# Kernel tuning notes

Measured on AMD Instinct MI355X. Metric: run time of the kernel, lower is better.

## Reference

```python
import jax, jax.numpy as jnp
import numpy as np

N, D, H, C = 100000, 128, 8, 16  # nodes, units=H*C, heads, per-head channels
E = 400000                        # edges per edge set (2 edge sets)
LN_EPS = 1e-3                     # keras LayerNormalization default epsilon


def setup_inputs() -> dict:
    key = jax.random.key(0)
    ks = jax.random.split(key, 16)
    def dense(k, i, o):
        return jax.random.normal(k, (i, o), jnp.float32) / np.float32(np.sqrt(i))
    return dict(
        x=jax.random.normal(ks[0], (N, D), jnp.float32),
        src0=jax.random.randint(ks[1], (E,), 0, N),
        dst0=jax.random.randint(ks[2], (E,), 0, N),
        src1=jax.random.randint(ks[3], (E,), 0, N),
        dst1=jax.random.randint(ks[4], (E,), 0, N),
        Wk=dense(ks[5], D, D), bk=jnp.zeros((D,), jnp.float32),
        Wm=dense(ks[6], D, D), bm=jnp.zeros((D,), jnp.float32),
        Wq=dense(ks[7], D, D), bq=jnp.zeros((D,), jnp.float32),
        Wa=dense(ks[8], D, D), ba=jnp.zeros((D,), jnp.float32),
        Watt0=jax.random.normal(ks[9], (H, C, C), jnp.float32) / np.float32(np.sqrt(C)),
        Wmsg0=jax.random.normal(ks[10], (H, C, C), jnp.float32) / np.float32(np.sqrt(C)),
        Watt1=jax.random.normal(ks[11], (H, C, C), jnp.float32) / np.float32(np.sqrt(C)),
        Wmsg1=jax.random.normal(ks[12], (H, C, C), jnp.float32) / np.float32(np.sqrt(C)),
        prior0=jnp.ones((H,), jnp.float32),
        prior1=jnp.ones((H,), jnp.float32),
        skip=jnp.ones((), jnp.float32),
        gamma=jnp.ones((D,), jnp.float32),
        beta=jnp.zeros((D,), jnp.float32),
    )


def reference(x, src0, dst0, src1, dst1, Wk, bk, Wm, bm, Wq, bq, Wa, ba,
              Watt0, Wmsg0, Watt1, Wmsg1, prior0, prior1, skip, gamma, beta):
    # Node-level projections, split per head: [N, H, C]
    k = (x @ Wk + bk).reshape(N, H, C)
    m = (x @ Wm + bm).reshape(N, H, C)
    q = (x @ Wq + bq).reshape(N, H, C)
    scale = 1.0 / jnp.sqrt(jnp.float32(C))

    def edge_terms(src, dst, Watt, Wmsg, prior):
        # per-edge-type relation projections of gathered sender keys/messages
        ke = jnp.einsum('ehk,hkl->ehl', k[src], Watt)          # [E, H, C]
        score = jnp.einsum('ehl,ehl->eh', ke, q[dst]) * prior * scale  # [E, H]
        msg = jnp.einsum('ehk,hkl->ehl', m[src], Wmsg)          # [E, H, C]
        return score, msg

    s0, m0 = edge_terms(src0, dst0, Watt0, Wmsg0, prior0)
    s1, m1 = edge_terms(src1, dst1, Watt1, Wmsg1, prior1)

    # Joint segment softmax over all incoming edges (both edge sets) per receiver
    scores = jnp.concatenate([s0, s1], axis=0)   # [2E, H]
    msgs = jnp.concatenate([m0, m1], axis=0)     # [2E, H, C]
    recv = jnp.concatenate([dst0, dst1], axis=0)

    smax = jax.ops.segment_max(scores, recv, num_segments=N)   # [N, H]
    ex = jnp.exp(scores - smax[recv])
    denom = jax.ops.segment_sum(ex, recv, num_segments=N)      # [N, H]
    d_e = denom[recv]
    attn = ex / jnp.where(d_e > 0, d_e, 1.0)                   # [2E, H]

    pooled = jax.ops.segment_sum(attn[:, :, None] * msgs, recv,
                                 num_segments=N).reshape(N, D)  # [N, D]

    # aggr(gelu(pooled)); weighted skip; layer norm
    h = jax.nn.gelu(pooled, approximate=False) @ Wa + ba
    alpha = jax.nn.sigmoid(skip)
    out = alpha * h + (1.0 - alpha) * x
    mu = jnp.mean(out, axis=-1, keepdims=True)
    var = jnp.var(out, axis=-1, keepdims=True)
    out = (out - mu) * jax.lax.rsqrt(var + LN_EPS) * gamma + beta
    return out
```

## Files before the change

kernel.cpp:

```cpp
#include <hip/hip_runtime.h>
#include <hip/hip_bf16.h>
#include <math.h>

#define N_NODES 100000
#define DIM 128
#define NH 8
#define NC 16
#define E_EDGES 400000
#define LN_EPS 1e-3f
#define SCAN_B 1024

typedef __attribute__((ext_vector_type(8))) short short8v;
typedef __attribute__((ext_vector_type(4))) short short4v;
typedef __attribute__((ext_vector_type(4))) float float4v;

__device__ __forceinline__ short bf16bits(float v) {
    __hip_bfloat16 b = __float2bfloat16(v);
    return *(short*)&b;
}

__global__ __launch_bounds__(128) void fuse_weights(
    const float* __restrict__ Wk, const float* __restrict__ bk,
    const float* __restrict__ Wm, const float* __restrict__ bm,
    const float* __restrict__ Wq, const float* __restrict__ bq,
    const float* __restrict__ Wa, const float* __restrict__ ba,
    const float* __restrict__ Watt0, const float* __restrict__ Wmsg0,
    const float* __restrict__ Watt1, const float* __restrict__ Wmsg1,
    const float* __restrict__ prior0, const float* __restrict__ prior1,
    __hip_bfloat16* __restrict__ Wt, float* __restrict__ bias)
{
    const int c = blockIdx.x;
    const int d = threadIdx.x;
    const int sec = c >> 7, j = c & 127, h = j >> 4, l = j & 15;
    float v, b;
    if (sec == 4)      { v = Wq[d * DIM + j]; b = bq[j]; }
    else if (sec == 5) { v = Wa[d * DIM + j]; b = ba[j]; }
    else {
        const float* W1 = (sec < 2) ? Wk : Wm;
        const float* bs = (sec < 2) ? bk : bm;
        const float* W2 = (sec == 0) ? Watt0 : (sec == 1) ? Watt1
                          : (sec == 2) ? Wmsg0 : Wmsg1;
        float scale = (sec == 0) ? prior0[h] * 0.25f
                    : (sec == 1) ? prior1[h] * 0.25f : 1.f;
        float s = 0.f, sb = 0.f;
        #pragma unroll
        for (int kk = 0; kk < NC; ++kk) {
            float w2 = W2[h * 256 + kk * 16 + l];
            s  = fmaf(W1[d * DIM + h * 16 + kk], w2, s);
            sb = fmaf(bs[h * 16 + kk], w2, sb);
        }
        v = s * scale; b = sb * scale;
    }
    Wt[(size_t)c * DIM + d] = __float2bfloat16(v);
    if (d == 0) bias[c] = b;
}

__global__ __launch_bounds__(256) void proj_mfma(
    const float* __restrict__ x,
    const __hip_bfloat16* __restrict__ Wt,
    const float* __restrict__ bias,
    __hip_bfloat16* __restrict__ kattC,
    __hip_bfloat16* __restrict__ mmsgC,
    __hip_bfloat16* __restrict__ qb)
{
    __shared__ __align__(16) short xs[32 * DIM];
    const int tid = threadIdx.x;
    const int wave = tid >> 6, lane = tid & 63;
    const int quad = lane >> 4, mcol = lane & 15;
    const int r0 = blockIdx.x * 32;

    {
        const int row = tid >> 3, c8 = tid & 7;
        const float* xp = x + (size_t)(r0 + row) * DIM + c8 * 16;
        float4v f[4];
        #pragma unroll
        for (int i = 0; i < 4; ++i) f[i] = *(const float4v*)(xp + i * 4);
        short8v s0, s1;
        #pragma unroll
        for (int j = 0; j < 8; ++j) {
            s0[j] = bf16bits(((const float*)f)[j]);
            s1[j] = bf16bits(((const float*)f)[j + 8]);
        }
        short* base = xs + row * DIM;
        *(short8v*)(base + (((2 * c8)     ^ (row & 7)) * 8)) = s0;
        *(short8v*)(base + (((2 * c8 + 1) ^ (row & 7)) * 8)) = s1;
    }
    __syncthreads();

    short8v b0[4], b1[4];
    #pragma unroll
    for (int kb = 0; kb < 4; ++kb) {
        const int ch = quad + kb * 4;
        b0[kb] = *(const short8v*)(xs + mcol * DIM + ((ch ^ (mcol & 7)) * 8));
        b1[kb] = *(const short8v*)(xs + (mcol + 16) * DIM + ((ch ^ (mcol & 7)) * 8));
    }

    #pragma unroll
    for (int s = 0; s < 5; ++s) {
        __hip_bfloat16* dst =
            (s == 0) ? kattC :
            (s == 1) ? kattC + (size_t)N_NODES * DIM :
            (s == 2) ? mmsgC :
            (s == 3) ? mmsgC + (size_t)N_NODES * DIM :
                       qb;
        short* drow0 = (short*)dst + (size_t)(r0 + mcol) * DIM;
        short* drow1 = drow0 + 16 * DIM;
        #pragma unroll
        for (int tp = 0; tp < 2; ++tp) {
            const int ct = (wave * 2 + tp) * 16;
            const int c0 = s * 128 + ct;
            const short* wp = (const short*)Wt + (size_t)(c0 + mcol) * DIM + quad * 8;
            float4v acc0 = {0.f, 0.f, 0.f, 0.f};
            float4v acc1 = {0.f, 0.f, 0.f, 0.f};
            #pragma unroll
            for (int kb = 0; kb < 4; ++kb) {
                short8v af = *(const short8v*)(wp + kb * 32);
                acc0 = __builtin_amdgcn_mfma_f32_16x16x32_bf16(af, b0[kb], acc0, 0, 0, 0);
                acc1 = __builtin_amdgcn_mfma_f32_16x16x32_bf16(af, b1[kb], acc1, 0, 0, 0);
            }
            const float4v b4 = *(const float4v*)(bias + c0 + quad * 4);
            short4v o0, o1;
            #pragma unroll
            for (int g = 0; g < 4; ++g) {
                o0[g] = bf16bits(acc0[g] + b4[g]);
                o1[g] = bf16bits(acc1[g] + b4[g]);
            }
            *(short4v*)(drow0 + ct + quad * 4) = o0;
            *(short4v*)(drow1 + ct + quad * 4) = o1;
        }
    }
}

__global__ __launch_bounds__(256) void hist_kernel(
    const int* __restrict__ dst0, const int* __restrict__ dst1,
    int* __restrict__ counts)
{
    int e = blockIdx.x * 256 + threadIdx.x;
    if (e < E_EDGES) atomicAdd(&counts[dst0[e]], 1);
    int e1 = e - E_EDGES;
    if (e1 >= 0 && e1 < E_EDGES) atomicAdd(&counts[dst1[e1]], 1);
}

__global__ __launch_bounds__(SCAN_B) void scanA_kernel(
    const int* __restrict__ counts, int* __restrict__ row_ptr,
    int* __restrict__ bsum)
{
    __shared__ int buf[2][SCAN_B];
    int i = blockIdx.x * SCAN_B + threadIdx.x;
    int v = (i < N_NODES) ? counts[i] : 0;
    int cur = 0;
    buf[0][threadIdx.x] = v;
    __syncthreads();
    #pragma unroll
    for (int off = 1; off < SCAN_B; off <<= 1) {
        int t = buf[cur][threadIdx.x];
        int add = (threadIdx.x >= off) ? buf[cur][threadIdx.x - off] : 0;
        buf[cur ^ 1][threadIdx.x] = t + add;
        cur ^= 1;
        __syncthreads();
    }
    int inc = buf[cur][threadIdx.x];
    if (i < N_NODES) row_ptr[i] = inc - v;
    if (threadIdx.x == SCAN_B - 1) bsum[blockIdx.x] = inc;
}

__global__ __launch_bounds__(128) void scanB_kernel(int* __restrict__ bsum, int nblocks)
{
    __shared__ int buf[2][128];
    int t = threadIdx.x;
    int v = (t < nblocks) ? bsum[t] : 0;
    buf[0][t] = v;
    __syncthreads();
    int cur = 0;
    #pragma unroll
    for (int off = 1; off < 128; off <<= 1) {
        int a = buf[cur][t];
        if (t >= off) a += buf[cur][t - off];
        buf[cur ^ 1][t] = a;
        cur ^= 1;
        __syncthreads();
    }
    if (t < nblocks) bsum[t] = buf[cur][t] - v;
}

__global__ __launch_bounds__(SCAN_B) void scanC_kernel(
    int* __restrict__ row_ptr, int* __restrict__ cursor,
    const int* __restrict__ bsum)
{
    int i = blockIdx.x * SCAN_B + threadIdx.x;
    if (i < N_NODES) {
        int r = row_ptr[i] + bsum[blockIdx.x];
        row_ptr[i] = r;
        cursor[i] = r;
    }
}

__global__ __launch_bounds__(256) void scatter_kernel(
    const int* __restrict__ src0, const int* __restrict__ dst0,
    const int* __restrict__ src1, const int* __restrict__ dst1,
    int* __restrict__ cursor, unsigned int* __restrict__ eidx)
{
    int e = blockIdx.x * 256 + threadIdx.x;
    if (e < E_EDGES) {
        int d = dst0[e];
        int pos = atomicAdd(&cursor[d], 1);
        eidx[pos] = (unsigned int)src0[e];
    }
    int e1 = e - E_EDGES;
    if (e1 >= 0 && e1 < E_EDGES) {
        int d = dst1[e1];
        int pos = atomicAdd(&cursor[d], 1);
        eidx[pos] = (unsigned int)(src1[e1] + N_NODES);
    }
}

__global__ __launch_bounds__(256) void agg_kernel(
    const __hip_bfloat162* __restrict__ katt,
    const __hip_bfloat162* __restrict__ mmsg,
    const __hip_bfloat162* __restrict__ qb2,
    const int* __restrict__ row_ptr, const int* __restrict__ counts,
    const unsigned int* __restrict__ eidx,
    __hip_bfloat162* __restrict__ pooled2)
{
    const int wave = threadIdx.x >> 6, lane = threadIdx.x & 63;
    const int n = blockIdx.x * 4 + wave;
    if (n >= N_NODES) return;
    const int start = row_ptr[n], cnt = counts[n];
    __hip_bfloat162 qv = qb2[(size_t)n * 64 + lane];
    const float qx = __bfloat162float(qv.x), qy = __bfloat162float(qv.y);

    float accx = 0.f, accy = 0.f, den = 0.f;
    int i = 0;
    for (; i + 2 <= cnt; i += 2) {
        unsigned int r0 = eidx[start + i];
        unsigned int r1 = eidx[start + i + 1];
        __hip_bfloat162 ka0 = katt[(size_t)r0 * 64 + lane];
        __hip_bfloat162 ka1 = katt[(size_t)r1 * 64 + lane];
        __hip_bfloat162 mg0 = mmsg[(size_t)r0 * 64 + lane];
        __hip_bfloat162 mg1 = mmsg[(size_t)r1 * 64 + lane];
        float p0 = fmaf(__bfloat162float(ka0.x), qx,
                        __bfloat162float(ka0.y) * qy);
        float p1 = fmaf(__bfloat162float(ka1.x), qx,
                        __bfloat162float(ka1.y) * qy);
        p0 += __shfl_xor(p0, 1, 64); p0 += __shfl_xor(p0, 2, 64); p0 += __shfl_xor(p0, 4, 64);
        p1 += __shfl_xor(p1, 1, 64); p1 += __shfl_xor(p1, 2, 64); p1 += __shfl_xor(p1, 4, 64);
        float e0 = __expf(p0), e1 = __expf(p1);
        accx = fmaf(e0, __bfloat162float(mg0.x), accx);
        accy = fmaf(e0, __bfloat162float(mg0.y), accy);
        accx = fmaf(e1, __bfloat162float(mg1.x), accx);
        accy = fmaf(e1, __bfloat162float(mg1.y), accy);
        den += e0 + e1;
    }
    if (i < cnt) {
        unsigned int r0 = eidx[start + i];
        __hip_bfloat162 ka0 = katt[(size_t)r0 * 64 + lane];
        __hip_bfloat162 mg0 = mmsg[(size_t)r0 * 64 + lane];
        float p0 = fmaf(__bfloat162float(ka0.x), qx,
                        __bfloat162float(ka0.y) * qy);
        p0 += __shfl_xor(p0, 1, 64); p0 += __shfl_xor(p0, 2, 64); p0 += __shfl_xor(p0, 4, 64);
        float e0 = __expf(p0);
        accx = fmaf(e0, __bfloat162float(mg0.x), accx);
        accy = fmaf(e0, __bfloat162float(mg0.y), accy);
        den += e0;
    }

    float vx = 0.f, vy = 0.f;
    if (den > 0.f) { vx = accx / den; vy = accy / den; }
    vx = 0.5f * vx * (1.f + erff(vx * 0.70710678118654752f));
    vy = 0.5f * vy * (1.f + erff(vy * 0.70710678118654752f));
    __hip_bfloat162 o; o.x = __float2bfloat16(vx); o.y = __float2bfloat16(vy);
    pooled2[(size_t)n * 64 + lane] = o;
}

__global__ __launch_bounds__(256) void final_mfma(
    const __hip_bfloat16* __restrict__ pooled,
    const __hip_bfloat16* __restrict__ Wt,
    const float* __restrict__ bias,
    const float* __restrict__ x,
    const float* __restrict__ skip, const float* __restrict__ gamma,
    const float* __restrict__ beta, float* __restrict__ out)
{
    __shared__ float hs[32][DIM];
    const int wave = threadIdx.x >> 6, lane = threadIdx.x & 63;
    const int quad = lane >> 4, mcol = lane & 15;
    const int r0 = blockIdx.x * 32;

    short8v a0[4], a1[4];
    const short* pp0 = (const short*)pooled + (size_t)(r0 + mcol) * DIM + quad * 8;
    const short* pp1 = pp0 + 16 * DIM;
    #pragma unroll
    for (int kb = 0; kb < 4; ++kb) {
        a0[kb] = *(const short8v*)(pp0 + kb * 32);
        a1[kb] = *(const short8v*)(pp1 + kb * 32);
    }
    const float alpha = 1.f / (1.f + expf(-skip[0]));

    #pragma unroll
    for (int t = 0; t < 2; ++t) {
        const int c0 = wave * 32 + t * 16;
        const short* wp = (const short*)Wt + (size_t)(640 + c0 + mcol) * DIM + quad * 8;
        float4v acc0 = {0.f, 0.f, 0.f, 0.f};
        float4v acc1 = {0.f, 0.f, 0.f, 0.f};
        #pragma unroll
        for (int kb = 0; kb < 4; ++kb) {
            short8v bfr = *(const short8v*)(wp + kb * 32);
            acc0 = __builtin_amdgcn_mfma_f32_16x16x32_bf16(a0[kb], bfr, acc0, 0, 0, 0);
            acc1 = __builtin_amdgcn_mfma_f32_16x16x32_bf16(a1[kb], bfr, acc1, 0, 0, 0);
        }
        const float bcol = bias[640 + c0 + mcol];
        const int cc = c0 + mcol;
        const int rq = quad * 4;
        #pragma unroll
        for (int g = 0; g < 4; ++g) {
            int rA = rq + g, rB = rq + 16 + g;
            hs[rA][cc] = alpha * (acc0[g] + bcol)
                       + (1.f - alpha) * x[(size_t)(r0 + rA) * DIM + cc];
            hs[rB][cc] = alpha * (acc1[g] + bcol)
                       + (1.f - alpha) * x[(size_t)(r0 + rB) * DIM + cc];
        }
    }
    __syncthreads();

    float gam0 = gamma[lane], gam1 = gamma[lane + 64];
    float bet0 = beta[lane],  bet1 = beta[lane + 64];
    for (int r = wave; r < 32; r += 4) {
        int row = r0 + r;
        float v0 = hs[r][lane], v1 = hs[r][lane + 64];
        float s = v0 + v1, s2 = v0 * v0 + v1 * v1;
        #pragma unroll
        for (int off = 1; off < 64; off <<= 1) {
            s  += __shfl_xor(s,  off, 64);
            s2 += __shfl_xor(s2, off, 64);
        }
        float mu = s * (1.f / 128.f);
        float var = s2 * (1.f / 128.f) - mu * mu;
        float rstd = rsqrtf(var + LN_EPS);
        out[(size_t)row * DIM + lane]      = (v0 - mu) * rstd * gam0 + bet0;
        out[(size_t)row * DIM + lane + 64] = (v1 - mu) * rstd * gam1 + bet1;
    }
}

extern "C" void kernel_launch(void* const* d_in, const int* in_sizes, int n_in,
                              void* d_out, int out_size, void* d_ws, size_t ws_size,
                              hipStream_t stream) {
    const float* x     = (const float*)d_in[0];
    const int*   src0  = (const int*)d_in[1];
    const int*   dst0  = (const int*)d_in[2];
    const int*   src1  = (const int*)d_in[3];
    const int*   dst1  = (const int*)d_in[4];
    const float* Wk    = (const float*)d_in[5];
    const float* bk    = (const float*)d_in[6];
    const float* Wm    = (const float*)d_in[7];
    const float* bm    = (const float*)d_in[8];
    const float* Wq    = (const float*)d_in[9];
    const float* bq    = (const float*)d_in[10];
    const float* Wa    = (const float*)d_in[11];
    const float* ba    = (const float*)d_in[12];
    const float* Watt0 = (const float*)d_in[13];
    const float* Wmsg0 = (const float*)d_in[14];
    const float* Watt1 = (const float*)d_in[15];
    const float* Wmsg1 = (const float*)d_in[16];
    const float* prior0= (const float*)d_in[17];
    const float* prior1= (const float*)d_in[18];
    const float* skip  = (const float*)d_in[19];
    const float* gamma = (const float*)d_in[20];
    const float* beta  = (const float*)d_in[21];
    float* out = (float*)d_out;

    const size_t nd = (size_t)N_NODES * DIM;
    char* wsb = (char*)d_ws;
    __hip_bfloat16* Wt    = (__hip_bfloat16*)wsb;  wsb += (size_t)768 * DIM * 2;
    float* bias           = (float*)wsb;           wsb += 768 * 4;
    __hip_bfloat16* kattC = (__hip_bfloat16*)wsb;  wsb += 2 * nd * 2;
    __hip_bfloat16* mmsgC = (__hip_bfloat16*)wsb;  wsb += 2 * nd * 2;
    __hip_bfloat16* qb    = (__hip_bfloat16*)wsb;  wsb += nd * 2;
    __hip_bfloat16* pooled= (__hip_bfloat16*)wsb;  wsb += nd * 2;
    int* counts  = (int*)wsb;                      wsb += (size_t)N_NODES * 4;
    int* row_ptr = (int*)wsb;                      wsb += (size_t)N_NODES * 4;
    int* cursor  = (int*)wsb;                      wsb += (size_t)N_NODES * 4;
    int* bsum    = (int*)wsb;                      wsb += 128 * 4;
    unsigned int* eidx = (unsigned int*)wsb;

    hipMemsetAsync(counts, 0, (size_t)N_NODES * 4, stream);

    const int scan_blocks = (N_NODES + SCAN_B - 1) / SCAN_B;
    const int edge_blocks = (2 * E_EDGES + 255) / 256;

    hist_kernel<<<dim3(edge_blocks), dim3(256), 0, stream>>>(dst0, dst1, counts);
    scanA_kernel<<<dim3(scan_blocks), dim3(SCAN_B), 0, stream>>>(counts, row_ptr, bsum);
    scanB_kernel<<<dim3(1), dim3(128), 0, stream>>>(bsum, scan_blocks);
    scanC_kernel<<<dim3(scan_blocks), dim3(SCAN_B), 0, stream>>>(row_ptr, cursor, bsum);
    scatter_kernel<<<dim3(edge_blocks), dim3(256), 0, stream>>>(
        src0, dst0, src1, dst1, cursor, eidx);

    fuse_weights<<<dim3(768), dim3(128), 0, stream>>>(
        Wk, bk, Wm, bm, Wq, bq, Wa, ba,
        Watt0, Wmsg0, Watt1, Wmsg1, prior0, prior1, Wt, bias);
    proj_mfma<<<dim3(N_NODES / 32), dim3(256), 0, stream>>>(
        x, Wt, bias, kattC, mmsgC, qb);

    agg_kernel<<<dim3((N_NODES + 3) / 4), dim3(256), 0, stream>>>(
        (const __hip_bfloat162*)kattC, (const __hip_bfloat162*)mmsgC,
        (const __hip_bfloat162*)qb, row_ptr, counts, eidx,
        (__hip_bfloat162*)pooled);

    final_mfma<<<dim3(N_NODES / 32), dim3(256), 0, stream>>>(
        pooled, Wt, bias, x, skip, gamma, beta, out);
}
```

Measured before the change: 408.9 us.

## Make projection kernel persistent with register-resident weights and double-buffered x tiles

Turns proj_mfma into a persistent kernel of 512 blocks with 8 waves each. Each wave keeps its slice of the fused weight matrix and bias in registers for all output sections, and the block loops over 32-row tiles. The next tile of x is prefetched into registers and written to a second LDS buffer while the current tile is computed, so global loads overlap with the MFMA work and weight reloads disappear. The cost is higher register pressure (weights held as 20 short8 vectors) and possibly lower occupancy. This kernel is also only one part of a larger pipeline whose time is probably dominated by the gather/aggregation step.

```diff
diff --git a/kernel.cpp b/kernel.cpp
--- a/kernel.cpp
+++ b/kernel.cpp
@@ -9,6 +9,7 @@
 #define E_EDGES 400000
 #define LN_EPS 1e-3f
 #define SCAN_B 1024
+#define PROJ_GRID 512
 
 typedef __attribute__((ext_vector_type(8))) short short8v;
 typedef __attribute__((ext_vector_type(4))) short short4v;
@@ -55,7 +56,7 @@
     if (d == 0) bias[c] = b;
 }
 
-__global__ __launch_bounds__(256) void proj_mfma(
+__global__ __launch_bounds__(512) void proj_mfma(
     const float* __restrict__ x,
     const __hip_bfloat16* __restrict__ Wt,
     const float* __restrict__ bias,
@@ -63,71 +64,98 @@
     __hip_bfloat16* __restrict__ mmsgC,
     __hip_bfloat16* __restrict__ qb)
 {
-    __shared__ __align__(16) short xs[32 * DIM];
+    __shared__ __align__(16) short xs[2][32 * DIM];
     const int tid = threadIdx.x;
     const int wave = tid >> 6, lane = tid & 63;
     const int quad = lane >> 4, mcol = lane & 15;
-    const int r0 = blockIdx.x * 32;
-
-    {
-        const int row = tid >> 3, c8 = tid & 7;
-        const float* xp = x + (size_t)(r0 + row) * DIM + c8 * 16;
-        float4v f[4];
-        #pragma unroll
-        for (int i = 0; i < 4; ++i) f[i] = *(const float4v*)(xp + i * 4);
-        short8v s0, s1;
-        #pragma unroll
-        for (int j = 0; j < 8; ++j) {
-            s0[j] = bf16bits(((const float*)f)[j]);
-            s1[j] = bf16bits(((const float*)f)[j + 8]);
-        }
-        short* base = xs + row * DIM;
-        *(short8v*)(base + (((2 * c8)     ^ (row & 7)) * 8)) = s0;
-        *(short8v*)(base + (((2 * c8 + 1) ^ (row & 7)) * 8)) = s1;
-    }
-    __syncthreads();
-
-    short8v b0[4], b1[4];
-    #pragma unroll
-    for (int kb = 0; kb < 4; ++kb) {
-        const int ch = quad + kb * 4;
-        b0[kb] = *(const short8v*)(xs + mcol * DIM + ((ch ^ (mcol & 7)) * 8));
-        b1[kb] = *(const short8v*)(xs + (mcol + 16) * DIM + ((ch ^ (mcol & 7)) * 8));
-    }
-
+    const int nt = N_NODES / 32;
+
+    short8v wf[5][4];
+    float4v bv[5];
     #pragma unroll
     for (int s = 0; s < 5; ++s) {
-        __hip_bfloat16* dst =
-            (s == 0) ? kattC :
-            (s == 1) ? kattC + (size_t)N_NODES * DIM :
-            (s == 2) ? mmsgC :
-            (s == 3) ? mmsgC + (size_t)N_NODES * DIM :
-                       qb;
-        short* drow0 = (short*)dst + (size_t)(r0 + mcol) * DIM;
-        short* drow1 = drow0 + 16 * DIM;
-        #pragma unroll
-        for (int tp = 0; tp < 2; ++tp) {
-            const int ct = (wave * 2 + tp) * 16;
-            const int c0 = s * 128 + ct;
-            const short* wp = (const short*)Wt + (size_t)(c0 + mcol) * DIM + quad * 8;
+        const int c0 = s * 128 + wave * 16;
+        const short* wp = (const short*)Wt + (size_t)(c0 + mcol) * DIM + quad * 8;
+        #pragma unroll
+        for (int kb = 0; kb < 4; ++kb)
+            wf[s][kb] = *(const short8v*)(wp + kb * 32);
+        bv[s] = *(const float4v*)(bias + c0 + quad * 4);
+    }
+
+    const int srow = tid >> 4, sc8 = tid & 15;
+    const int swz = ((sc8 ^ (srow & 7)) * 8);
+
+    int t = blockIdx.x;
+    if (t >= nt) return;
+
+    float4v f0 = *(const float4v*)(x + (size_t)(t * 32 + srow) * DIM + sc8 * 8);
+    float4v f1 = *(const float4v*)(x + (size_t)(t * 32 + srow) * DIM + sc8 * 8 + 4);
+    {
+        short8v sv;
+        #pragma unroll
+        for (int j = 0; j < 4; ++j) { sv[j] = bf16bits(f0[j]); sv[j + 4] = bf16bits(f1[j]); }
+        *(short8v*)(xs[0] + srow * DIM + swz) = sv;
+    }
+    {
+        int nn = t + PROJ_GRID;
+        if (nn < nt) {
+            f0 = *(const float4v*)(x + (size_t)(nn * 32 + srow) * DIM + sc8 * 8);
+            f1 = *(const float4v*)(x + (size_t)(nn * 32 + srow) * DIM + sc8 * 8 + 4);
+        }
+    }
+
+    int cur = 0;
+    for (; t < nt; t += PROJ_GRID) {
+        __syncthreads();
+
+        short8v b0[4], b1[4];
+        #pragma unroll
+        for (int kb = 0; kb < 4; ++kb) {
+            const int ch = ((quad + kb * 4) ^ (mcol & 7)) * 8;
+            b0[kb] = *(const short8v*)(xs[cur] + mcol * DIM + ch);
+            b1[kb] = *(const short8v*)(xs[cur] + (mcol + 16) * DIM + ch);
+        }
+
+        const int r0 = t * 32;
+        #pragma unroll
+        for (int s = 0; s < 5; ++s) {
             float4v acc0 = {0.f, 0.f, 0.f, 0.f};
             float4v acc1 = {0.f, 0.f, 0.f, 0.f};
             #pragma unroll
             for (int kb = 0; kb < 4; ++kb) {
-                short8v af = *(const short8v*)(wp + kb * 32);
-                acc0 = __builtin_amdgcn_mfma_f32_16x16x32_bf16(af, b0[kb], acc0, 0, 0, 0);
-                acc1 = __builtin_amdgcn_mfma_f32_16x16x32_bf16(af, b1[kb], acc1, 0, 0, 0);
+                acc0 = __builtin_amdgcn_mfma_f32_16x16x32_bf16(wf[s][kb], b0[kb], acc0, 0, 0, 0);
+                acc1 = __builtin_amdgcn_mfma_f32_16x16x32_bf16(wf[s][kb], b1[kb], acc1, 0, 0, 0);
             }
-            const float4v b4 = *(const float4v*)(bias + c0 + quad * 4);
+            __hip_bfloat16* dst =
+                (s == 0) ? kattC :
+                (s == 1) ? kattC + (size_t)N_NODES * DIM :
+                (s == 2) ? mmsgC :
+                (s == 3) ? mmsgC + (size_t)N_NODES * DIM :
+                           qb;
+            short* drow0 = (short*)dst + (size_t)(r0 + mcol) * DIM + wave * 16 + quad * 4;
             short4v o0, o1;
             #pragma unroll
             for (int g = 0; g < 4; ++g) {
-                o0[g] = bf16bits(acc0[g] + b4[g]);
-                o1[g] = bf16bits(acc1[g] + b4[g]);
+                o0[g] = bf16bits(acc0[g] + bv[s][g]);
+                o1[g] = bf16bits(acc1[g] + bv[s][g]);
             }
-            *(short4v*)(drow0 + ct + quad * 4) = o0;
-            *(short4v*)(drow1 + ct + quad * 4) = o1;
-        }
+            *(short4v*)drow0              = o0;
+            *(short4v*)(drow0 + 16 * DIM) = o1;
+        }
+
+        int nn = t + PROJ_GRID;
+        if (nn < nt) {
+            short8v sv;
+            #pragma unroll
+            for (int j = 0; j < 4; ++j) { sv[j] = bf16bits(f0[j]); sv[j + 4] = bf16bits(f1[j]); }
+            *(short8v*)(xs[cur ^ 1] + srow * DIM + swz) = sv;
+            int n2 = nn + PROJ_GRID;
+            if (n2 < nt) {
+                f0 = *(const float4v*)(x + (size_t)(n2 * 32 + srow) * DIM + sc8 * 8);
+                f1 = *(const float4v*)(x + (size_t)(n2 * 32 + srow) * DIM + sc8 * 8 + 4);
+            }
+        }
+        cur ^= 1;
     }
 }
 
@@ -396,7 +424,7 @@
     fuse_weights<<<dim3(768), dim3(128), 0, stream>>>(
         Wk, bk, Wm, bm, Wq, bq, Wa, ba,
         Watt0, Wmsg0, Watt1, Wmsg1, prior0, prior1, Wt, bias);
-    proj_mfma<<<dim3(N_NODES / 32), dim3(256), 0, stream>>>(
+    proj_mfma<<<dim3(PROJ_GRID), dim3(512), 0, stream>>>(
         x, Wt, bias, kattC, mmsgC, qb);
 
     agg_kernel<<<dim3((N_NODES + 3) / 4), dim3(256), 0, stream>>>(
```

Result: faster. 372.9 us (-8.8%).
